# Kernel optimization log

Measured on AMD Instinct MI355X. Metric: run time of the kernel, lower is better.

The kernel has to match this reference:

```python
import jax, jax.numpy as jnp
import numpy as np

EPS_W = 1e-9


def area2d(a, b, c):
    # signed parallelogram area; a/b/c are [..., >=2] points
    return (b[..., 0] - a[..., 0]) * (c[..., 1] - a[..., 1]) - (b[..., 1] - a[..., 1]) * (c[..., 0] - a[..., 0])


def lookup_table(size):
    # square table of 2d points (x, y) in [-1, 1], matching torch meshgrid('ij') + rot90
    lin = jnp.linspace(-1.0, 1.0, size, dtype=jnp.float32)
    xx, yy = jnp.meshgrid(lin, lin, indexing='ij')
    t = jnp.stack([xx, yy], axis=-1)
    return jnp.rot90(t, 1, axes=(0, 1))  # [S,S,2]


def grid_sample_bilinear(img, grid):
    # img [C,H,W]; grid [...,2] with (x,y) in [-1,1]; bilinear, zero padding, align_corners=True
    C, H, W = img.shape
    x, y = grid[..., 0], grid[..., 1]
    ix = (x + 1.0) * (W - 1) * 0.5
    iy = (y + 1.0) * (H - 1) * 0.5
    ix0 = jnp.floor(ix)
    iy0 = jnp.floor(iy)
    ix1 = ix0 + 1.0
    iy1 = iy0 + 1.0
    wx1 = ix - ix0
    wx0 = 1.0 - wx1
    wy1 = iy - iy0
    wy0 = 1.0 - wy1

    def tap(iyf, ixf):
        inb = (ixf >= 0) & (ixf <= W - 1) & (iyf >= 0) & (iyf <= H - 1)
        ii = jnp.clip(ixf, 0, W - 1).astype(jnp.int32)
        jj = jnp.clip(iyf, 0, H - 1).astype(jnp.int32)
        return img[:, jj, ii] * inb.astype(img.dtype)  # [C, ...]

    return (tap(iy0, ix0) * (wy0 * wx0) + tap(iy0, ix1) * (wy0 * wx1)
            + tap(iy1, ix0) * (wy1 * wx0) + tap(iy1, ix1) * (wy1 * wx1))


def _render(vertices, uv, uvmap, faces, uvfaces, size):
    pts = lookup_table(size)              # [S,S,2]
    uvn = uv * 2.0 - 1.0                  # uv scaled to [-1,1] as in __init__
    tris = vertices[faces]                # [K,3,3]
    uvt = uvn[uvfaces]                    # [K,3,2]

    # backface cull mask (z-component of cross(v1-v0, v2-v0) > 0)
    e1 = tris[:, 1] - tris[:, 0]
    e2 = tris[:, 2] - tris[:, 0]
    normal_z = e1[:, 0] * e2[:, 1] - e1[:, 1] * e2[:, 0]
    valid = normal_z > 0

    zinit = jnp.min(vertices, axis=0)[-1]
    result0 = jnp.zeros((4, size, size), jnp.float32)
    zbuf0 = jnp.full((size, size), zinit, dtype=jnp.float32)

    def step(carry, xs):
        result, zbuf = carry
        tri, uvtri, ok = xs               # tri [3,3], uvtri [3,2], ok scalar bool
        tri2d = tri[:, :2]
        w = area2d(tri2d[0], tri2d[1], tri2d[2])
        # sub areas against every pixel (dense equivalent of AABB + inside masks)
        pAB = area2d(tri2d[1], pts, tri2d[0])   # [S,S]
        pCB = area2d(tri2d[2], pts, tri2d[1])
        pCA = area2d(tri2d[0], pts, tri2d[2])
        inside = (pAB > 0) & (pCB > 0) & (pCA > 0)
        ws = jnp.where(w >= EPS_W, w, 1.0)      # safe divide; masked out below
        w1 = pCB / ws
        w2 = pCA / ws
        w3 = 1.0 - w1 - w2
        z = w1 * tri[0, 2] + w2 * tri[1, 2] + w3 * tri[2, 2]   # [S,S]
        mask = ok & (w >= EPS_W) & inside & (z >= zbuf)
        # barycentric uv interpolation + bilinear texture lookup
        ptsUV = w1[..., None] * uvtri[0] + w2[..., None] * uvtri[1] + w3[..., None] * uvtri[2]  # [S,S,2]
        rgb = grid_sample_bilinear(uvmap, ptsUV)  # [3,S,S]
        zbuf = jnp.where(mask, z, zbuf)
        rgba = jnp.concatenate([rgb, jnp.ones((1, size, size), result.dtype)], axis=0)
        result = jnp.where(mask[None], rgba, result)
        return (result, zbuf), None

    (result, _), _ = jax.lax.scan(step, (result0, zbuf0), (tris, uvt, valid))
    return result


def setup_inputs() -> dict:
    key = jax.random.key(0)
    k0, k1, k2, k3, k4 = jax.random.split(key, 5)
    V, K, M, T, S = 1500, 1500, 2000, 1024, 512
    vertices = jax.random.normal(k0, (V, 3), dtype=jnp.float32)
    faces = jax.random.randint(k1, (K, 3), 0, V)
    uv = jax.random.uniform(k2, (M, 2), dtype=jnp.float32)
    uvfaces = jax.random.randint(k3, (K, 3), 0, M)
    uvmap = jax.random.normal(k4, (3, T, T), dtype=jnp.float32)
    return {"vertices": vertices, "faces": faces, "uv": uv,
            "uvfaces": uvfaces, "uvmap": uvmap, "size": S}


def reference(vertices, faces, uv, uvfaces, uvmap, size):
    return _render(vertices, uv, uvmap, faces, uvfaces, size)
```

## Files before the change

### kernel.cpp

```cpp
#include <hip/hip_runtime.h>
#include <hip/hip_fp16.h>
#include <cmath>

#pragma clang fp contract(off)

#define MAXK 2048

struct TriUV {
  float u0x, u0y, u1x, u1y;
  float u2x, u2y, pad0, pad1;
};

__device__ __forceinline__ float h2f(unsigned v) {
  __half_raw r; r.x = (unsigned short)v;
  return __half2float(__half(r));
}
__device__ __forceinline__ unsigned f2h(float v) {
  return (unsigned)__half_as_ushort(__float2half(v));
}
__device__ __forceinline__ unsigned pkh(float lo, float hi) {
  return f2h(lo) | (f2h(hi) << 16);
}
__device__ __forceinline__ unsigned fmapu(float f) {
  unsigned b = __float_as_uint(f);
  return (b & 0x80000000u) ? ~b : (b | 0x80000000u);
}
__device__ __forceinline__ float funmap(unsigned m) {
  return __uint_as_float((m & 0x80000000u) ? (m ^ 0x80000000u) : ~m);
}

__device__ __forceinline__ float lin_at(int i, int n) {
#pragma clang fp contract(off)
  if (i == n - 1) return 1.0f;
  float step = (float)i / (float)(n - 1);
  return (-1.0f) * (1.0f - step) + 1.0f * step;
}

__global__ __launch_bounds__(256) void prep_kernel(
    const float* __restrict__ verts, const int* __restrict__ faces,
    const float* __restrict__ uv, const int* __restrict__ uvfaces, int V, int K,
    float4* __restrict__ q0S, float4* __restrict__ q1S,
    float4* __restrict__ q2S, float4* __restrict__ q3S,
    float4* __restrict__ bboxS, uint4* __restrict__ apS,
    float4* __restrict__ metaS, float4* __restrict__ planeS,
    TriUV* __restrict__ tuv, float* __restrict__ zinit) {
#pragma clang fp contract(off)
  __shared__ float smz[256];
  int tid = (int)threadIdx.x;
  int bid = (int)blockIdx.x;
  if (bid == 0) {
    float m = 3.402823466e38f;
    for (int i = tid; i < V; i += 256) m = fminf(m, verts[3 * i + 2]);
    smz[tid] = m;
    __syncthreads();
    for (int s2 = 128; s2 > 0; s2 >>= 1) {
      if (tid < s2) smz[tid] = fminf(smz[tid], smz[tid + s2]);
      __syncthreads();
    }
    if (tid == 0) *zinit = smz[0];
    return;
  }
  int t = (bid - 1) * 256 + tid;
  if (t >= K) return;
  int i0 = faces[3 * t + 0], i1 = faces[3 * t + 1], i2 = faces[3 * t + 2];
  float t0x = verts[3 * i0 + 0], t0y = verts[3 * i0 + 1], z0 = verts[3 * i0 + 2];
  float t1x = verts[3 * i1 + 0], t1y = verts[3 * i1 + 1], z1 = verts[3 * i1 + 2];
  float t2x = verts[3 * i2 + 0], t2y = verts[3 * i2 + 1], z2 = verts[3 * i2 + 2];
  int j0 = uvfaces[3 * t + 0], j1 = uvfaces[3 * t + 1], j2 = uvfaces[3 * t + 2];
  TriUV u;
  u.u0x = uv[2 * j0 + 0] * 2.0f - 1.0f;
  u.u0y = uv[2 * j0 + 1] * 2.0f - 1.0f;
  u.u1x = uv[2 * j1 + 0] * 2.0f - 1.0f;
  u.u1y = uv[2 * j1 + 1] * 2.0f - 1.0f;
  u.u2x = uv[2 * j2 + 0] * 2.0f - 1.0f;
  u.u2y = uv[2 * j2 + 1] * 2.0f - 1.0f;
  u.pad0 = 0.0f; u.pad1 = 0.0f;
  tuv[t] = u;
  float w = (t1x - t0x) * (t2y - t0y) - (t1y - t0y) * (t2x - t0x);
  if (w < 1e-9f) {
    bboxS[t] = make_float4(3.0e38f, -3.0e38f, 3.0e38f, -3.0e38f);
    return;
  }
  float dAy = t0y - t1y, dAx = t0x - t1x;
  float dBy = t1y - t2y, dBx = t1x - t2x;
  float dCy = t2y - t0y, dCx = t2x - t0x;
  q0S[t] = make_float4(t1x, t1y, dAy, dAx);
  q1S[t] = make_float4(t2x, t2y, dBy, dBx);
  q2S[t] = make_float4(t0x, t0y, dCy, dCx);
  q3S[t] = make_float4(z0, z1, z2, w);
  bboxS[t] = make_float4(fminf(fminf(t0x, t1x), t2x),
                         fmaxf(fmaxf(t0x, t1x), t2x),
                         fminf(fminf(t0y, t1y), t2y),
                         fmaxf(fmaxf(t0y, t1y), t2y));
  float fA = t1y * dAx - t1x * dAy;
  float fB = t2y * dBx - t2x * dBy;
  float fC = t0y * dCx - t0x * dCy;
  float sA = fabsf(dAy) + fabsf(dAx) + fabsf(fA);
  float sB = fabsf(dBy) + fabsf(dBx) + fabsf(fB);
  float sC = fabsf(dCy) + fabsf(dCx) + fabsf(fC);
  float M = fmaxf(fmaxf(sA, sB), sC) * 9.766e-4f + 1e-4f;
  apS[t] = make_uint4(pkh(dAy, dAx), pkh(fA, dBy), pkh(dBx, fB),
                      pkh(dCy, dCx));
  metaS[t] = make_float4(M, fC, __int_as_float(t), 0.0f);
  float zmx = fmaxf(fmaxf(z0, z1), z2);
  float gatef = zmx + 1e-3f + 1e-4f / w;
  float gx = (z0 * dBy + z1 * dCy + z2 * dAy) / w;
  float gy = -(z0 * dBx + z1 * dCx + z2 * dAx) / w;
  float cc = (z0 * fB + z1 * fC + z2 * fA) / w;
  float mm = (fabsf(z0 * fB) + fabsf(z1 * fC) + fabsf(z2 * fA) +
              fabsf(z0 * dBy) + fabsf(z1 * dCy) + fabsf(z2 * dAy) +
              fabsf(z0 * dBx) + fabsf(z1 * dCx) + fabsf(z2 * dAx)) *
                 (2e-6f / w) +
             1e-3f + 1e-4f / w + 1e-4f;
  planeS[t] = make_float4(gx, gy, cc + mm, gatef);
}

__global__ __launch_bounds__(1024) void render_kernel(
    const float4* __restrict__ q0S, const float4* __restrict__ q1S,
    const float4* __restrict__ q2S, const float4* __restrict__ q3S,
    const float4* __restrict__ bboxS, const uint4* __restrict__ apS,
    const float4* __restrict__ metaS, const float4* __restrict__ planeS,
    int N, const TriUV* __restrict__ tuv, const float* __restrict__ zinitp,
    const float* __restrict__ uvmap, int T, float* __restrict__ out, int S) {
#pragma clang fp contract(off)
  __shared__ unsigned short s_kept[MAXK];
  __shared__ unsigned s_tgm[MAXK];
  __shared__ unsigned s_em[MAXK];
  __shared__ unsigned long long s_key[256];
  __shared__ unsigned s_zu[256];
  __shared__ unsigned s_hist[256];
  __shared__ int s_cur[256];
  __shared__ unsigned s_wsum[4];

  int tid = (int)threadIdx.x;
  int wv = tid >> 6, ln = tid & 63;
  int s = wv >> 2, q = wv & 3;
  int pix = (q << 6) + ln;
  int tilesX = S >> 4;
  int tileX = (int)blockIdx.x % tilesX;
  int tileY = (int)blockIdx.x / tilesX;
  int j = (tileX << 4) + (pix & 15);
  int i = (tileY << 4) + (pix >> 4);
  float px = lin_at(j, S);
  float py = lin_at(S - 1 - i, S);
  float pxlo = lin_at(tileX << 4, S);
  float pxhi = lin_at((tileX << 4) + 15, S);
  float pylo = lin_at(S - 1 - ((tileY << 4) + 15), S);
  float pyhi = lin_at(S - 1 - (tileY << 4), S);

  float zinit = *zinitp;
  unsigned zinit_m = fmapu(zinit);
  if (tid < 256) {
    s_zu[tid] = zinit_m;
    s_key[tid] = ((unsigned long long)zinit_m << 32);
    s_hist[tid] = 0u;
  }
  volatile unsigned* vzu = s_zu;
  __syncthreads();

  bool kA = false, kB = false;
  int bA = 0, bB = 0;
  unsigned gA = 0, gB = 0;
  {
    int t = tid;
    if (t < N) {
      float4 bb = bboxS[t];
      if (bb.x <= pxhi && bb.y >= pxlo && bb.z <= pyhi && bb.w >= pylo) {
        float4 pl = planeS[t];
        float ub = pl.z + fmaxf(pl.x * pxlo, pl.x * pxhi) +
                   fmaxf(pl.y * pylo, pl.y * pyhi);
        float tg = fminf(pl.w, ub);
        kA = true;
        bA = min(max((int)((4.0f - tg) * 32.0f), 0), 255);
        gA = fmapu(tg);
      }
    }
    t = tid + 1024;
    if (t < N) {
      float4 bb = bboxS[t];
      if (bb.x <= pxhi && bb.y >= pxlo && bb.z <= pyhi && bb.w >= pylo) {
        float4 pl = planeS[t];
        float ub = pl.z + fmaxf(pl.x * pxlo, pl.x * pxhi) +
                   fmaxf(pl.y * pylo, pl.y * pyhi);
        float tg = fminf(pl.w, ub);
        kB = true;
        bB = min(max((int)((4.0f - tg) * 32.0f), 0), 255);
        gB = fmapu(tg);
      }
    }
  }
  if (kA) atomicAdd(&s_hist[bA], 1u);
  if (kB) atomicAdd(&s_hist[bB], 1u);
  __syncthreads();
  unsigned hx = 0, hinc = 0;
  if (tid < 256) {
    hx = s_hist[tid];
    unsigned v = hx;
#pragma unroll
    for (int d = 1; d < 64; d <<= 1) {
      unsigned tv = __shfl_up(v, d, 64);
      if (ln >= d) v += tv;
    }
    if (ln == 63) s_wsum[wv] = v;
    hinc = v;
  }
  __syncthreads();
  if (tid < 256) {
    unsigned add = 0;
    for (int w2 = 0; w2 < wv; ++w2) add += s_wsum[w2];
    hinc += add;
    s_hist[tid] = hinc;
    s_cur[tid] = (int)(hinc - hx);
  }
  __syncthreads();
  int nk = (int)s_hist[255];
  if (kA) {
    int sl = atomicAdd(&s_cur[bA], 1);
    s_kept[sl] = (unsigned short)tid;
    s_tgm[sl] = gA;
    float ef = (bA == 0) ? 3.402823466e38f : (4.0f - (float)bA * 0.03125f);
    s_em[sl] = fmapu(ef);
  }
  if (kB) {
    int sl = atomicAdd(&s_cur[bB], 1);
    s_kept[sl] = (unsigned short)(tid + 1024);
    s_tgm[sl] = gB;
    float ef = (bB == 0) ? 3.402823466e38f : (4.0f - (float)bB * 0.03125f);
    s_em[sl] = fmapu(ef);
  }
  __syncthreads();

  for (int a = s; a < nk; a += 4) {
    unsigned em = s_em[a];
    unsigned zb = vzu[pix];
    if (__all(em < zb)) break;
    if (em >= zb && s_tgm[a] >= zb) {
      int idx = s_kept[a];
      uint4 ap = apS[idx];
      float4 mt = metaS[idx];
      float M = mt.x, fC = mt.y;
      float aA = fmaf(px, h2f(ap.x & 0xffffu),
                      fmaf(-py, h2f(ap.x >> 16), h2f(ap.y & 0xffffu)));
      float aB = fmaf(px, h2f(ap.y >> 16),
                      fmaf(-py, h2f(ap.z & 0xffffu), h2f(ap.z >> 16)));
      float aC = fmaf(px, h2f(ap.w & 0xffffu),
                      fmaf(-py, h2f(ap.w >> 16), fC));
      if (fminf(fminf(aA, aB), aC) > -M) {
        float4 q0 = q0S[idx], q1 = q1S[idx], q2 = q2S[idx];
        float pAB = (px - q0.x) * q0.z - (py - q0.y) * q0.w;
        float pCB = (px - q1.x) * q1.z - (py - q1.y) * q1.w;
        float pCA = (px - q2.x) * q2.z - (py - q2.y) * q2.w;
        if (pAB > 0.0f && pCB > 0.0f && pCA > 0.0f) {
          float4 q3 = q3S[idx];
          float w = q3.w;
          float bzf = funmap(vzu[pix]);
          float zs = (pCB * q3.x + pCA * q3.y) + ((w - pCB) - pCA) * q3.z;
          if (w < 1e-3f || zs >= (bzf - 1e-3f) * w) {
            float w1 = pCB / w;
            float w2 = pCA / w;
            float w3 = (1.0f - w1) - w2;
            float z = (w1 * q3.x + w2 * q3.y) + w3 * q3.z;
            int o = __float_as_int(mt.z);
            unsigned zm = fmapu(z);
            unsigned long long key =
                ((unsigned long long)zm << 32) | (unsigned)(o + 1);
            atomicMax(&s_key[pix], key);
            atomicMax(&s_zu[pix], zm);
          }
        }
      }
    }
  }
  __syncthreads();

  if (tid < 256) {
    unsigned long long key = s_key[tid];
    unsigned oP1 = (unsigned)(key & 0xFFFFFFFFULL);
    float o0 = 0.0f, o1 = 0.0f, o2 = 0.0f, o3 = 0.0f;
    if (oP1 != 0) {
      int o = (int)oP1 - 1;
      float4 q1 = q1S[o], q2 = q2S[o], q3 = q3S[o];
      float pCB = (px - q1.x) * q1.z - (py - q1.y) * q1.w;
      float pCA = (px - q2.x) * q2.z - (py - q2.y) * q2.w;
      float w1 = pCB / q3.w;
      float w2 = pCA / q3.w;
      float w3 = (1.0f - w1) - w2;
      TriUV u = tuv[o];
      float x = (w1 * u.u0x + w2 * u.u1x) + w3 * u.u2x;
      float y = (w1 * u.u0y + w2 * u.u1y) + w3 * u.u2y;
      float WH = (float)(T - 1);
      float fx = ((x + 1.0f) * WH) * 0.5f;
      float fy = ((y + 1.0f) * WH) * 0.5f;
      float ix0 = floorf(fx), iy0 = floorf(fy);
      float ix1 = ix0 + 1.0f, iy1 = iy0 + 1.0f;
      float wx1 = fx - ix0, wx0 = 1.0f - wx1;
      float wy1 = fy - iy0, wy0 = 1.0f - wy1;
      float w00 = wy0 * wx0, w01 = wy0 * wx1;
      float w10 = wy1 * wx0, w11 = wy1 * wx1;
      bool bx0 = (ix0 >= 0.0f) && (ix0 <= WH);
      bool bx1 = (ix1 >= 0.0f) && (ix1 <= WH);
      bool by0 = (iy0 >= 0.0f) && (iy0 <= WH);
      bool by1 = (iy1 >= 0.0f) && (iy1 <= WH);
      float m00 = (by0 && bx0) ? 1.0f : 0.0f;
      float m01 = (by0 && bx1) ? 1.0f : 0.0f;
      float m10 = (by1 && bx0) ? 1.0f : 0.0f;
      float m11 = (by1 && bx1) ? 1.0f : 0.0f;
      int cx0 = (int)fminf(fmaxf(ix0, 0.0f), WH);
      int cx1 = (int)fminf(fmaxf(ix1, 0.0f), WH);
      int cy0 = (int)fminf(fmaxf(iy0, 0.0f), WH);
      int cy1 = (int)fminf(fmaxf(iy1, 0.0f), WH);
      int TT = T * T;
      int i00 = cy0 * T + cx0, i01 = cy0 * T + cx1;
      int i10 = cy1 * T + cx0, i11 = cy1 * T + cx1;
      {
        const float* img = uvmap;
        float v00 = img[i00] * m00, v01 = img[i01] * m01;
        float v10 = img[i10] * m10, v11 = img[i11] * m11;
        o0 = ((v00 * w00 + v01 * w01) + v10 * w10) + v11 * w11;
      }
      {
        const float* img = uvmap + TT;
        float v00 = img[i00] * m00, v01 = img[i01] * m01;
        float v10 = img[i10] * m10, v11 = img[i11] * m11;
        o1 = ((v00 * w00 + v01 * w01) + v10 * w10) + v11 * w11;
      }
      {
        const float* img = uvmap + 2 * TT;
        float v00 = img[i00] * m00, v01 = img[i01] * m01;
        float v10 = img[i10] * m10, v11 = img[i11] * m11;
        o2 = ((v00 * w00 + v01 * w01) + v10 * w10) + v11 * w11;
      }
      o3 = 1.0f;
    }
    int p = i * S + j;
    int SS = S * S;
    out[p] = o0;
    out[SS + p] = o1;
    out[2 * SS + p] = o2;
    out[3 * SS + p] = o3;
  }
}

extern "C" void kernel_launch(void* const* d_in, const int* in_sizes, int n_in,
                              void* d_out, int out_size, void* d_ws,
                              size_t ws_size, hipStream_t stream) {
  const float* verts = (const float*)d_in[0];
  const int* faces = (const int*)d_in[1];
  const float* uv = (const float*)d_in[2];
  const int* uvfaces = (const int*)d_in[3];
  const float* uvmap = (const float*)d_in[4];
  int V = in_sizes[0] / 3;
  int K = in_sizes[1] / 3;
  int T = (int)lroundf(sqrtf((float)(in_sizes[4] / 3)));
  int S = (int)lroundf(sqrtf((float)(out_size / 4)));
  float* outp = (float*)d_out;

  char* ws = (char*)d_ws;
  size_t off = 0;
  auto alloc = [&](size_t bytes) {
    void* p = ws + off;
    off = (off + bytes + 255) & ~(size_t)255;
    return p;
  };
  float* zinit = (float*)alloc(4);
  float4* q0S = (float4*)alloc((size_t)MAXK * 16);
  float4* q1S = (float4*)alloc((size_t)MAXK * 16);
  float4* q2S = (float4*)alloc((size_t)MAXK * 16);
  float4* q3S = (float4*)alloc((size_t)MAXK * 16);
  float4* bboxS = (float4*)alloc((size_t)MAXK * 16);
  uint4* apS = (uint4*)alloc((size_t)MAXK * 16);
  float4* metaS = (float4*)alloc((size_t)MAXK * 16);
  float4* planeS = (float4*)alloc((size_t)MAXK * 16);
  TriUV* tuv = (TriUV*)alloc((size_t)K * sizeof(TriUV));

  int pblocks = 1 + (K + 255) / 256;
  prep_kernel<<<pblocks, 256, 0, stream>>>(verts, faces, uv, uvfaces, V, K,
                                           q0S, q1S, q2S, q3S, bboxS, apS,
                                           metaS, planeS, tuv, zinit);
  int tiles = (S >> 4) * (S >> 4);
  render_kernel<<<tiles, 1024, 0, stream>>>(q0S, q1S, q2S, q3S, bboxS, apS,
                                            metaS, planeS, K, tuv, zinit,
                                            uvmap, T, outp, S);
}
```

Before: 32.57 us.

## Pack per-triangle data into one 128-byte record and merge LDS candidate arrays

Moves the separate per-triangle arrays (ap, meta, q0..q3) into a single 128-byte aligned struct, so one triangle's data sits in one cache line instead of six scattered lines. The three shared-memory candidate arrays are merged into one uint4 array, so a single LDS load yields the depth bound, gate and index. The redundant em>=zb test is dropped from the per-candidate condition. The cost is more LDS use (32KB for the candidate list) and padding bytes in global memory, and the larger shared footprint may reduce occupancy.

```diff
diff --git a/kernel.cpp b/kernel.cpp
--- a/kernel.cpp
+++ b/kernel.cpp
@@ -9,6 +9,16 @@
 struct TriUV {
   float u0x, u0y, u1x, u1y;
   float u2x, u2y, pad0, pad1;
+};
+
+struct __align__(128) TriRec {
+  uint4 ap;
+  float4 mt;
+  float4 q0;
+  float4 q1;
+  float4 q2;
+  float4 q3;
+  float4 pad0, pad1;
 };
 
 __device__ __forceinline__ float h2f(unsigned v) {
@@ -39,11 +49,9 @@
 __global__ __launch_bounds__(256) void prep_kernel(
     const float* __restrict__ verts, const int* __restrict__ faces,
     const float* __restrict__ uv, const int* __restrict__ uvfaces, int V, int K,
-    float4* __restrict__ q0S, float4* __restrict__ q1S,
-    float4* __restrict__ q2S, float4* __restrict__ q3S,
-    float4* __restrict__ bboxS, uint4* __restrict__ apS,
-    float4* __restrict__ metaS, float4* __restrict__ planeS,
-    TriUV* __restrict__ tuv, float* __restrict__ zinit) {
+    TriRec* __restrict__ rec, float4* __restrict__ bboxS,
+    float4* __restrict__ planeS, TriUV* __restrict__ tuv,
+    float* __restrict__ zinit) {
 #pragma clang fp contract(off)
   __shared__ float smz[256];
   int tid = (int)threadIdx.x;
@@ -84,10 +92,6 @@
   float dAy = t0y - t1y, dAx = t0x - t1x;
   float dBy = t1y - t2y, dBx = t1x - t2x;
   float dCy = t2y - t0y, dCx = t2x - t0x;
-  q0S[t] = make_float4(t1x, t1y, dAy, dAx);
-  q1S[t] = make_float4(t2x, t2y, dBy, dBx);
-  q2S[t] = make_float4(t0x, t0y, dCy, dCx);
-  q3S[t] = make_float4(z0, z1, z2, w);
   bboxS[t] = make_float4(fminf(fminf(t0x, t1x), t2x),
                          fmaxf(fmaxf(t0x, t1x), t2x),
                          fminf(fminf(t0y, t1y), t2y),
@@ -99,9 +103,16 @@
   float sB = fabsf(dBy) + fabsf(dBx) + fabsf(fB);
   float sC = fabsf(dCy) + fabsf(dCx) + fabsf(fC);
   float M = fmaxf(fmaxf(sA, sB), sC) * 9.766e-4f + 1e-4f;
-  apS[t] = make_uint4(pkh(dAy, dAx), pkh(fA, dBy), pkh(dBx, fB),
-                      pkh(dCy, dCx));
-  metaS[t] = make_float4(M, fC, __int_as_float(t), 0.0f);
+  TriRec r;
+  r.ap = make_uint4(pkh(dAy, dAx), pkh(fA, dBy), pkh(dBx, fB), pkh(dCy, dCx));
+  r.mt = make_float4(M, fC, __int_as_float(t), 0.0f);
+  r.q0 = make_float4(t1x, t1y, dAy, dAx);
+  r.q1 = make_float4(t2x, t2y, dBy, dBx);
+  r.q2 = make_float4(t0x, t0y, dCy, dCx);
+  r.q3 = make_float4(z0, z1, z2, w);
+  r.pad0 = make_float4(0.f, 0.f, 0.f, 0.f);
+  r.pad1 = make_float4(0.f, 0.f, 0.f, 0.f);
+  rec[t] = r;
   float zmx = fmaxf(fmaxf(z0, z1), z2);
   float gatef = zmx + 1e-3f + 1e-4f / w;
   float gx = (z0 * dBy + z1 * dCy + z2 * dAy) / w;
@@ -116,16 +127,12 @@
 }
 
 __global__ __launch_bounds__(1024) void render_kernel(
-    const float4* __restrict__ q0S, const float4* __restrict__ q1S,
-    const float4* __restrict__ q2S, const float4* __restrict__ q3S,
-    const float4* __restrict__ bboxS, const uint4* __restrict__ apS,
-    const float4* __restrict__ metaS, const float4* __restrict__ planeS,
-    int N, const TriUV* __restrict__ tuv, const float* __restrict__ zinitp,
-    const float* __restrict__ uvmap, int T, float* __restrict__ out, int S) {
+    const TriRec* __restrict__ rec, const float4* __restrict__ bboxS,
+    const float4* __restrict__ planeS, int N, const TriUV* __restrict__ tuv,
+    const float* __restrict__ zinitp, const float* __restrict__ uvmap, int T,
+    float* __restrict__ out, int S) {
 #pragma clang fp contract(off)
-  __shared__ unsigned short s_kept[MAXK];
-  __shared__ unsigned s_tgm[MAXK];
-  __shared__ unsigned s_em[MAXK];
+  __shared__ uint4 s_g[MAXK];
   __shared__ unsigned long long s_key[256];
   __shared__ unsigned s_zu[256];
   __shared__ unsigned s_hist[256];
@@ -216,28 +223,24 @@
   int nk = (int)s_hist[255];
   if (kA) {
     int sl = atomicAdd(&s_cur[bA], 1);
-    s_kept[sl] = (unsigned short)tid;
-    s_tgm[sl] = gA;
     float ef = (bA == 0) ? 3.402823466e38f : (4.0f - (float)bA * 0.03125f);
-    s_em[sl] = fmapu(ef);
+    s_g[sl] = make_uint4(fmapu(ef), gA, (unsigned)tid, 0u);
   }
   if (kB) {
     int sl = atomicAdd(&s_cur[bB], 1);
-    s_kept[sl] = (unsigned short)(tid + 1024);
-    s_tgm[sl] = gB;
     float ef = (bB == 0) ? 3.402823466e38f : (4.0f - (float)bB * 0.03125f);
-    s_em[sl] = fmapu(ef);
+    s_g[sl] = make_uint4(fmapu(ef), gB, (unsigned)(tid + 1024), 0u);
   }
   __syncthreads();
 
   for (int a = s; a < nk; a += 4) {
-    unsigned em = s_em[a];
+    uint4 g = s_g[a];
     unsigned zb = vzu[pix];
-    if (__all(em < zb)) break;
-    if (em >= zb && s_tgm[a] >= zb) {
-      int idx = s_kept[a];
-      uint4 ap = apS[idx];
-      float4 mt = metaS[idx];
+    if (__all(g.x < zb)) break;
+    if (g.y >= zb) {
+      const TriRec* r = &rec[g.z];
+      uint4 ap = r->ap;
+      float4 mt = r->mt;
       float M = mt.x, fC = mt.y;
       float aA = fmaf(px, h2f(ap.x & 0xffffu),
                       fmaf(-py, h2f(ap.x >> 16), h2f(ap.y & 0xffffu)));
@@ -246,12 +249,12 @@
       float aC = fmaf(px, h2f(ap.w & 0xffffu),
                       fmaf(-py, h2f(ap.w >> 16), fC));
       if (fminf(fminf(aA, aB), aC) > -M) {
-        float4 q0 = q0S[idx], q1 = q1S[idx], q2 = q2S[idx];
+        float4 q0 = r->q0, q1 = r->q1, q2 = r->q2;
         float pAB = (px - q0.x) * q0.z - (py - q0.y) * q0.w;
         float pCB = (px - q1.x) * q1.z - (py - q1.y) * q1.w;
         float pCA = (px - q2.x) * q2.z - (py - q2.y) * q2.w;
         if (pAB > 0.0f && pCB > 0.0f && pCA > 0.0f) {
-          float4 q3 = q3S[idx];
+          float4 q3 = r->q3;
           float w = q3.w;
           float bzf = funmap(vzu[pix]);
           float zs = (pCB * q3.x + pCA * q3.y) + ((w - pCB) - pCA) * q3.z;
@@ -279,7 +282,8 @@
     float o0 = 0.0f, o1 = 0.0f, o2 = 0.0f, o3 = 0.0f;
     if (oP1 != 0) {
       int o = (int)oP1 - 1;
-      float4 q1 = q1S[o], q2 = q2S[o], q3 = q3S[o];
+      const TriRec* r = &rec[o];
+      float4 q1 = r->q1, q2 = r->q2, q3 = r->q3;
       float pCB = (px - q1.x) * q1.z - (py - q1.y) * q1.w;
       float pCA = (px - q2.x) * q2.z - (py - q2.y) * q2.w;
       float w1 = pCB / q3.w;
@@ -363,22 +367,15 @@
     return p;
   };
   float* zinit = (float*)alloc(4);
-  float4* q0S = (float4*)alloc((size_t)MAXK * 16);
-  float4* q1S = (float4*)alloc((size_t)MAXK * 16);
-  float4* q2S = (float4*)alloc((size_t)MAXK * 16);
-  float4* q3S = (float4*)alloc((size_t)MAXK * 16);
+  TriRec* rec = (TriRec*)alloc((size_t)MAXK * sizeof(TriRec));
   float4* bboxS = (float4*)alloc((size_t)MAXK * 16);
-  uint4* apS = (uint4*)alloc((size_t)MAXK * 16);
-  float4* metaS = (float4*)alloc((size_t)MAXK * 16);
   float4* planeS = (float4*)alloc((size_t)MAXK * 16);
   TriUV* tuv = (TriUV*)alloc((size_t)K * sizeof(TriUV));
 
   int pblocks = 1 + (K + 255) / 256;
   prep_kernel<<<pblocks, 256, 0, stream>>>(verts, faces, uv, uvfaces, V, K,
-                                           q0S, q1S, q2S, q3S, bboxS, apS,
-                                           metaS, planeS, tuv, zinit);
+                                           rec, bboxS, planeS, tuv, zinit);
   int tiles = (S >> 4) * (S >> 4);
-  render_kernel<<<tiles, 1024, 0, stream>>>(q0S, q1S, q2S, q3S, bboxS, apS,
-                                            metaS, planeS, K, tuv, zinit,
+  render_kernel<<<tiles, 1024, 0, stream>>>(rec, bboxS, planeS, K, tuv, zinit,
                                             uvmap, T, outp, S);
 }
```

New measurement: 31.79 us. -2.4%, faster.
